# Kernel optimization log

Hardware: AMD Instinct MI355X
Metric: run time of the kernel (lower is better)

## Reference

```python
import jax, jax.numpy as jnp
import numpy as np

D_MODEL = 2048
H_TOTAL = 32
D_HEAD = D_MODEL // H_TOTAL  # 64
H_ACTIVE = 4
ROPE_BASE = 10000.0


def _apply_rope(t, cos, sin):
    # t: [B, H, T, DH]; cos/sin: [T, DH//2]; interleaved pair rotation
    t1 = t[..., 0::2]
    t2 = t[..., 1::2]
    r1 = t1 * cos - t2 * sin
    r2 = t1 * sin + t2 * cos
    return jnp.stack([r1, r2], axis=-1).reshape(t.shape)


def setup_inputs() -> dict:
    key = jax.random.key(0)
    ks = jax.random.split(key, 4)
    x = jax.random.normal(ks[0], (4, 1024, D_MODEL), dtype=jnp.float32)
    w_router = jax.random.normal(ks[1], (D_MODEL, H_TOTAL), dtype=jnp.float32) * 0.02
    w_qkv = jax.random.normal(ks[2], (D_MODEL, 3 * D_MODEL), dtype=jnp.float32) * 0.02
    w_out = jax.random.normal(ks[3], (D_MODEL, D_MODEL), dtype=jnp.float32) * 0.02
    return {"x": x, "w_router": w_router, "w_qkv": w_qkv, "w_out": w_out}


def reference(x, w_router, w_qkv, w_out):
    B, T, _ = x.shape
    # --- SwitchRouter: per-token probabilities over heads ---
    probs = jax.nn.softmax(x @ w_router, axis=-1)            # [B, T, H]
    # top-h_active heads per token (dense-math equivalent of sparse dispatch)
    _, top_idx = jax.lax.top_k(probs, H_ACTIVE)              # [B, T, HA]
    mask = jnp.sum(jax.nn.one_hot(top_idx, H_TOTAL, dtype=x.dtype), axis=-2)  # [B, T, H]
    gate = probs * mask                                      # router-scored gate

    # --- QKV projection ---
    qkv = x @ w_qkv                                          # [B, T, 3D]
    q, k, v = jnp.split(qkv, 3, axis=-1)
    def to_heads(t):
        return t.reshape(B, T, H_TOTAL, D_HEAD).transpose(0, 2, 1, 3)  # [B, H, T, DH]
    q, k, v = to_heads(q), to_heads(k), to_heads(v)

    # --- RoPE ---
    inv_freq = 1.0 / (ROPE_BASE ** (jnp.arange(0, D_HEAD, 2, dtype=jnp.float32) / D_HEAD))
    ang = jnp.arange(T, dtype=jnp.float32)[:, None] * inv_freq[None, :]  # [T, DH/2]
    cos, sin = jnp.cos(ang), jnp.sin(ang)
    q = _apply_rope(q, cos, sin)
    k = _apply_rope(k, cos, sin)

    # --- causal SDPA ---
    scores = jnp.einsum('bhqd,bhkd->bhqk', q, k) / np.float32(np.sqrt(D_HEAD))
    causal = jnp.tril(jnp.ones((T, T), dtype=bool))
    scores = jnp.where(causal, scores, jnp.finfo(scores.dtype).min)
    attn = jax.nn.softmax(scores, axis=-1)
    out = jnp.einsum('bhqk,bhkd->bhqd', attn, v)             # [B, H, T, DH]

    # --- gate: only active heads contribute (scatter-back equivalent) ---
    out = out * gate.transpose(0, 2, 1)[..., None]           # [B, H, T, DH]
    out = out.transpose(0, 2, 1, 3).reshape(B, T, D_MODEL)
    return out @ w_out
```

## Files before the change

kernel.cpp:

```cpp
#include <hip/hip_runtime.h>
#include <hip/hip_bf16.h>
#include <stdint.h>
#include <stddef.h>

typedef __attribute__((ext_vector_type(8))) short bf16x8;
typedef __attribute__((ext_vector_type(8))) unsigned short u16x8;
typedef __attribute__((ext_vector_type(4))) float f32x4;

#define TT 1024

__device__ __forceinline__ unsigned short f2bf(float f){
  unsigned u = __builtin_bit_cast(unsigned, f);
  unsigned r = 0x7fffu + ((u >> 16) & 1u);
  return (unsigned short)((u + r) >> 16);
}
__device__ __forceinline__ float bf2f(unsigned short s){
  unsigned u = ((unsigned)s) << 16;
  return __builtin_bit_cast(float, u);
}
__device__ __forceinline__ void gload16(const unsigned short* g, unsigned short* l){
  __builtin_amdgcn_global_load_lds(
      (const __attribute__((address_space(1))) void*)g,
      (__attribute__((address_space(3))) void*)l, 16, 0, 0);
}

__global__ void transpose_cast_kernel(const float* __restrict__ in, unsigned short* __restrict__ out,
                                      int R, int C){
  __shared__ float tile[32][33];
  int c0 = blockIdx.x * 32, r0 = blockIdx.y * 32;
  for (int i = threadIdx.y; i < 32; i += 8)
    tile[i][threadIdx.x] = in[(size_t)(r0 + i) * C + c0 + threadIdx.x];
  __syncthreads();
  for (int i = threadIdx.y; i < 32; i += 8)
    out[(size_t)(c0 + i) * R + r0 + threadIdx.x] = f2bf(tile[threadIdx.x][i]);
}

__global__ void rope_table_kernel(float* __restrict__ tab){
  int idx = blockIdx.x * 256 + threadIdx.x;
  int pos = idx >> 5, i = idx & 31;
  float freq = powf(10000.0f, -(float)i / 32.0f);
  float ang = (float)pos * freq;
  tab[idx * 2]     = cosf(ang);
  tab[idx * 2 + 1] = sinf(ang);
}

__global__ __launch_bounds__(256) void prep_kernel(const float* __restrict__ x,
                                                   const float* __restrict__ wr,
                                                   unsigned short* __restrict__ x_bf,
                                                   float* __restrict__ gate){
  __shared__ float xc[8 * 256];
  __shared__ float red[8 * 8 * 32];
  const int tid = threadIdx.x;
  const int tok0 = blockIdx.x * 8;
  const int p = tid >> 5, h = tid & 31;
  float acc[8] = {0.f,0.f,0.f,0.f,0.f,0.f,0.f,0.f};

  for (int kb = 0; kb < 8; kb++){
    __syncthreads();
    {
      int tok = tid >> 5, e = (tid & 31) * 8;
      const float* xp = x + (size_t)(tok0 + tok) * 2048 + kb * 256 + e;
      float4 v0 = *(const float4*)xp, v1 = *(const float4*)(xp + 4);
      float vals[8] = {v0.x, v0.y, v0.z, v0.w, v1.x, v1.y, v1.z, v1.w};
      u16x8 ob;
      #pragma unroll
      for (int jj = 0; jj < 8; jj++) ob[jj] = f2bf(vals[jj]);
      *(u16x8*)(x_bf + (size_t)(tok0 + tok) * 2048 + kb * 256 + e) = ob;
      #pragma unroll
      for (int jj = 0; jj < 8; jj++) xc[tok * 256 + e + jj] = vals[jj];
    }
    __syncthreads();
    const float* wp = wr + (size_t)(kb * 256 + p * 32) * 32 + h;
    #pragma unroll 4
    for (int j = 0; j < 32; j++){
      float wv = wp[j * 32];
      #pragma unroll
      for (int tok = 0; tok < 8; tok++)
        acc[tok] += xc[tok * 256 + p * 32 + j] * wv;
    }
  }
  #pragma unroll
  for (int tok = 0; tok < 8; tok++) red[(p * 8 + tok) * 32 + h] = acc[tok];
  __syncthreads();

  {
    int lane = tid & 63;
    int tok = (tid >> 6) * 2 + (lane >> 5);
    int hh = lane & 31;
    float logit = 0.f;
    #pragma unroll
    for (int pp = 0; pp < 8; pp++) logit += red[(pp * 8 + tok) * 32 + hh];
    float m = logit;
    #pragma unroll
    for (int s = 16; s >= 1; s >>= 1) m = fmaxf(m, __shfl_xor(m, s));
    float e = __expf(logit - m);
    float sum = e;
    #pragma unroll
    for (int s = 16; s >= 1; s >>= 1) sum += __shfl_xor(sum, s);
    float prob = e / sum;
    float v = logit; int sel = 0;
    #pragma unroll
    for (int rr2 = 0; rr2 < 4; rr2++){
      float bv = v; int bi = hh;
      #pragma unroll
      for (int s = 16; s >= 1; s >>= 1){
        float ov = __shfl_xor(bv, s); int oi = __shfl_xor(bi, s);
        if (ov > bv || (ov == bv && oi < bi)) { bv = ov; bi = oi; }
      }
      if (hh == bi) { sel = 1; v = -3.4e38f; }
    }
    gate[(size_t)(tok0 + tok) * 32 + hh] = sel ? prob : 0.f;
  }
}

__global__ void compact_kernel(const float* __restrict__ gate, int* __restrict__ idx,
                               int* __restrict__ counts){
  int bh = blockIdx.x;
  int b = bh >> 5, h = bh & 31;
  int lane = threadIdx.x;
  int base = 0;
  for (int c = 0; c < 16; c++){
    int t = c * 64 + lane;
    bool act = gate[(size_t)(b * TT + t) * 32 + h] != 0.f;
    unsigned long long mask = __ballot(act);
    int pos = base + __popcll(mask & ((1ull << lane) - 1ull));
    if (act) idx[bh * TT + pos] = t;
    base += __popcll(mask);
  }
  if (lane == 0) counts[bh] = base;
}

__global__ __launch_bounds__(256) void gemm_qkv(const unsigned short* __restrict__ A,
                                                const unsigned short* __restrict__ Bt,
                                                unsigned short* __restrict__ qk,
                                                unsigned short* __restrict__ vt,
                                                const float* __restrict__ tab){
  __shared__ unsigned short As[3][128 * 32];
  __shared__ unsigned short Bs[3][128 * 32];
  const int K = 2048;
  const int bn = blockIdx.x, bm = blockIdx.y;
  const int tid = threadIdx.x, lane = tid & 63, wid = tid >> 6;
  const int wr = wid >> 1, wc = wid & 1;
  const int li = lane & 15, lg = lane >> 4;

  const unsigned short* gA0 = A  + (size_t)(bm * 128 + (tid >> 2)) * K + (tid & 3) * 8;
  const unsigned short* gA1 = gA0 + (size_t)64 * K;
  const unsigned short* gB0 = Bt + (size_t)(bn * 128 + (tid >> 2)) * K + (tid & 3) * 8;
  const unsigned short* gB1 = gB0 + (size_t)64 * K;

  f32x4 acc[4][4];
  #pragma unroll
  for (int i = 0; i < 4; i++)
    #pragma unroll
    for (int j = 0; j < 4; j++) acc[i][j] = f32x4{0.f, 0.f, 0.f, 0.f};

  const int NT = K >> 5;
  #pragma unroll
  for (int pp = 0; pp < 2; pp++){
    int ko = pp * 32;
    gload16(gA0 + ko, &As[pp][tid * 8]);
    gload16(gA1 + ko, &As[pp][(256 + tid) * 8]);
    gload16(gB0 + ko, &Bs[pp][tid * 8]);
    gload16(gB1 + ko, &Bs[pp][(256 + tid) * 8]);
  }
  for (int t = 0; t < NT; ++t){
    if (t == NT - 1) asm volatile("s_waitcnt vmcnt(0)" ::: "memory");
    else             asm volatile("s_waitcnt vmcnt(4)" ::: "memory");
    __builtin_amdgcn_s_barrier();
    __builtin_amdgcn_sched_barrier(0);
    const int sl = t % 3;
    const unsigned short* as = &As[sl][0];
    const unsigned short* bs = &Bs[sl][0];
    bf16x8 af[4], bfr[4];
    #pragma unroll
    for (int i = 0; i < 4; i++){
      af[i]  = *(const bf16x8*)(as + (wr * 64 + i * 16 + li) * 32 + lg * 8);
      bfr[i] = *(const bf16x8*)(bs + (wc * 64 + i * 16 + li) * 32 + lg * 8);
    }
    if (t + 2 < NT){
      const int s2 = (t + 2) % 3;
      const int ko = (t + 2) * 32;
      gload16(gA0 + ko, &As[s2][tid * 8]);
      gload16(gA1 + ko, &As[s2][(256 + tid) * 8]);
      gload16(gB0 + ko, &Bs[s2][tid * 8]);
      gload16(gB1 + ko, &Bs[s2][(256 + tid) * 8]);
    }
    #pragma unroll
    for (int i = 0; i < 4; i++)
      #pragma unroll
      for (int j = 0; j < 4; j++)
        acc[i][j] = __builtin_amdgcn_mfma_f32_16x16x32_bf16(af[i], bfr[j], acc[i][j], 0, 0, 0);
  }

  if (bn < 32){
    #pragma unroll
    for (int i = 0; i < 4; i++){
      #pragma unroll
      for (int j = 0; j < 4; j++){
        int col = bn * 128 + wc * 64 + j * 16 + li;
        int ii = (col & 63) >> 1;
        #pragma unroll
        for (int r = 0; r < 4; r++){
          int row = bm * 128 + wr * 64 + i * 16 + lg * 4 + r;
          int pos = row & (TT - 1);
          const float* tp = tab + ((size_t)pos * 32 + ii) * 2;
          float c = tp[0], s = tp[1];
          float val = acc[i][j][r];
          float pv = __shfl_xor(val, 1);
          float res = (li & 1) ? (pv * s + val * c) : (val * c - pv * s);
          qk[(size_t)row * 4096 + col] = f2bf(res);
        }
      }
    }
  } else {
    #pragma unroll
    for (int i = 0; i < 4; i++){
      #pragma unroll
      for (int j = 0; j < 4; j++){
        int vcol = bn * 128 + wc * 64 + j * 16 + li - 4096;
        int hh = vcol >> 6, d = vcol & 63;
        int row0 = bm * 128 + wr * 64 + i * 16 + lg * 4;
        int b = row0 >> 10, t0 = row0 & (TT - 1);
        ushort4 pk;
        pk.x = f2bf(acc[i][j][0]); pk.y = f2bf(acc[i][j][1]);
        pk.z = f2bf(acc[i][j][2]); pk.w = f2bf(acc[i][j][3]);
        *(ushort4*)(vt + ((size_t)((b * 32 + hh) * 64 + d)) * TT + t0) = pk;
      }
    }
  }
}

__global__ __launch_bounds__(256) void gemm_out(const unsigned short* __restrict__ A,
                                                const unsigned short* __restrict__ Bt,
                                                float* __restrict__ C,
                                                int M, int N, int K){
  __shared__ unsigned short As[3][128 * 32];
  __shared__ unsigned short Bs[3][128 * 32];
  const int bn = blockIdx.x, bm = blockIdx.y;
  const int tid = threadIdx.x, lane = tid & 63, wid = tid >> 6;
  const int wr = wid >> 1, wc = wid & 1;
  const int li = lane & 15, lg = lane >> 4;
  const unsigned short* gA0 = A  + (size_t)(bm * 128 + (tid >> 2)) * K + (tid & 3) * 8;
  const unsigned short* gA1 = gA0 + (size_t)64 * K;
  const unsigned short* gB0 = Bt + (size_t)(bn * 128 + (tid >> 2)) * K + (tid & 3) * 8;
  const unsigned short* gB1 = gB0 + (size_t)64 * K;
  f32x4 acc[4][4];
  #pragma unroll
  for (int i = 0; i < 4; i++)
    #pragma unroll
    for (int j = 0; j < 4; j++) acc[i][j] = f32x4{0.f, 0.f, 0.f, 0.f};
  const int NT = K >> 5;
  #pragma unroll
  for (int pp = 0; pp < 2; pp++){
    int ko = pp * 32;
    gload16(gA0 + ko, &As[pp][tid * 8]);
    gload16(gA1 + ko, &As[pp][(256 + tid) * 8]);
    gload16(gB0 + ko, &Bs[pp][tid * 8]);
    gload16(gB1 + ko, &Bs[pp][(256 + tid) * 8]);
  }
  for (int t = 0; t < NT; ++t){
    if (t == NT - 1) asm volatile("s_waitcnt vmcnt(0)" ::: "memory");
    else             asm volatile("s_waitcnt vmcnt(4)" ::: "memory");
    __builtin_amdgcn_s_barrier();
    __builtin_amdgcn_sched_barrier(0);
    const int sl = t % 3;
    const unsigned short* as = &As[sl][0];
    const unsigned short* bs = &Bs[sl][0];
    bf16x8 af[4], bfr[4];
    #pragma unroll
    for (int i = 0; i < 4; i++){
      af[i]  = *(const bf16x8*)(as + (wr * 64 + i * 16 + li) * 32 + lg * 8);
      bfr[i] = *(const bf16x8*)(bs + (wc * 64 + i * 16 + li) * 32 + lg * 8);
    }
    if (t + 2 < NT){
      const int s2 = (t + 2) % 3;
      const int ko = (t + 2) * 32;
      gload16(gA0 + ko, &As[s2][tid * 8]);
      gload16(gA1 + ko, &As[s2][(256 + tid) * 8]);
      gload16(gB0 + ko, &Bs[s2][tid * 8]);
      gload16(gB1 + ko, &Bs[s2][(256 + tid) * 8]);
    }
    #pragma unroll
    for (int i = 0; i < 4; i++)
      #pragma unroll
      for (int j = 0; j < 4; j++)
        acc[i][j] = __builtin_amdgcn_mfma_f32_16x16x32_bf16(af[i], bfr[j], acc[i][j], 0, 0, 0);
  }
  #pragma unroll
  for (int i = 0; i < 4; i++)
    #pragma unroll
    for (int j = 0; j < 4; j++)
      #pragma unroll
      for (int r = 0; r < 4; r++){
        size_t row = (size_t)(bm * 128 + wr * 64 + i * 16 + lg * 4 + r);
        size_t col = (size_t)(bn * 128 + wc * 64 + j * 16 + li);
        C[row * N + col] = acc[i][j][r];
      }
}

__global__ __launch_bounds__(256) void attn_sparse_kernel(const unsigned short* __restrict__ qk,
                                                          const unsigned short* __restrict__ vt,
                                                          const float* __restrict__ gate,
                                                          const int* __restrict__ idx,
                                                          const int* __restrict__ counts,
                                                          unsigned short* __restrict__ attn_out){
  __shared__ unsigned short Ks[64 * 64];
  __shared__ unsigned short Vs[64 * 64];
  __shared__ unsigned short Ps[4][16 * 64];
  const int bh = blockIdx.x, qt = blockIdx.y;
  const int count = counts[bh];
  if (qt * 64 >= count) return;
  const int b = bh >> 5, h = bh & 31;
  const int tid = threadIdx.x, lane = tid & 63, w = tid >> 6;
  const int li = lane & 15, lg = lane >> 4;
  const int* myidx = idx + bh * TT + qt * 64;
  const int nvalid = min(64, count - qt * 64);
  const int qmax = myidx[nvalid - 1];

  int qi[4];
  #pragma unroll
  for (int r = 0; r < 4; r++){
    int s = w * 16 + lg * 4 + r;
    qi[r] = (s < nvalid) ? myidx[s] : -1;
  }
  int qrow = (w * 16 + li < nvalid) ? myidx[w * 16 + li] : 0;
  bf16x8 qf0, qf1;
  {
    const unsigned short* qp = qk + (size_t)(b * TT + qrow) * 4096 + h * 64;
    qf0 = *(const bf16x8*)(qp + lg * 8);
    qf1 = *(const bf16x8*)(qp + 32 + lg * 8);
  }
  f32x4 o[4];
  #pragma unroll
  for (int i = 0; i < 4; i++) o[i] = f32x4{0.f, 0.f, 0.f, 0.f};
  float m_run[4], l_run[4];
  #pragma unroll
  for (int r = 0; r < 4; r++){ m_run[r] = -1e30f; l_run[r] = 0.f; }

  const int nkt = (qmax >> 6) + 1;
  for (int kt = 0; kt < nkt; kt++){
    const int kb = kt * 64;
    #pragma unroll
    for (int s2 = 0; s2 < 2; s2++){
      int s = s2 * 256 + tid;
      int r = s >> 3, c = (s & 7) * 8;
      gload16(qk + (size_t)(b * TT + kb + r) * 4096 + 2048 + h * 64 + c, &Ks[s * 8]);
      gload16(vt + (size_t)(bh * 64 + r) * TT + kb + c, &Vs[s * 8]);
    }
    __syncthreads();

    f32x4 s4[4];
    #pragma unroll
    for (int ni = 0; ni < 4; ni++){
      bf16x8 k0 = *(const bf16x8*)(&Ks[(ni * 16 + li) * 64 + lg * 8]);
      bf16x8 k1 = *(const bf16x8*)(&Ks[(ni * 16 + li) * 64 + 32 + lg * 8]);
      f32x4 t = f32x4{0.f, 0.f, 0.f, 0.f};
      t = __builtin_amdgcn_mfma_f32_16x16x32_bf16(qf0, k0, t, 0, 0, 0);
      t = __builtin_amdgcn_mfma_f32_16x16x32_bf16(qf1, k1, t, 0, 0, 0);
      s4[ni] = t;
    }
    float mt[4];
    #pragma unroll
    for (int r = 0; r < 4; r++) mt[r] = -1e30f;
    #pragma unroll
    for (int ni = 0; ni < 4; ni++){
      int kidx = kb + ni * 16 + li;
      #pragma unroll
      for (int r = 0; r < 4; r++){
        float val = s4[ni][r] * 0.125f;
        val = (kidx <= qi[r]) ? val : -1e30f;
        s4[ni][r] = val;
        mt[r] = fmaxf(mt[r], val);
      }
    }
    #pragma unroll
    for (int r = 0; r < 4; r++){
      #pragma unroll
      for (int sh = 8; sh >= 1; sh >>= 1) mt[r] = fmaxf(mt[r], __shfl_xor(mt[r], sh));
      float mnew = fmaxf(m_run[r], mt[r]);
      float corr = __expf(m_run[r] - mnew);
      m_run[r] = mnew;
      l_run[r] *= corr;
      #pragma unroll
      for (int j = 0; j < 4; j++) o[j][r] *= corr;
    }
    float rs[4] = {0.f, 0.f, 0.f, 0.f};
    #pragma unroll
    for (int ni = 0; ni < 4; ni++)
      #pragma unroll
      for (int r = 0; r < 4; r++){
        float p = __expf(s4[ni][r] - m_run[r]);
        s4[ni][r] = p;
        rs[r] += p;
      }
    #pragma unroll
    for (int r = 0; r < 4; r++){
      #pragma unroll
      for (int sh = 8; sh >= 1; sh >>= 1) rs[r] += __shfl_xor(rs[r], sh);
      l_run[r] += rs[r];
    }
    #pragma unroll
    for (int ni = 0; ni < 4; ni++)
      #pragma unroll
      for (int r = 0; r < 4; r++)
        Ps[w][(lg * 4 + r) * 64 + ni * 16 + li] = f2bf(s4[ni][r]);
    #pragma unroll
    for (int ks = 0; ks < 2; ks++){
      bf16x8 pa = *(const bf16x8*)(&Ps[w][li * 64 + ks * 32 + lg * 8]);
      #pragma unroll
      for (int ni = 0; ni < 4; ni++){
        bf16x8 vb = *(const bf16x8*)(&Vs[(ni * 16 + li) * 64 + ks * 32 + lg * 8]);
        o[ni] = __builtin_amdgcn_mfma_f32_16x16x32_bf16(pa, vb, o[ni], 0, 0, 0);
      }
    }
    __syncthreads();
  }
  #pragma unroll
  for (int r = 0; r < 4; r++){
    if (qi[r] < 0) continue;
    float g = gate[(size_t)(b * TT + qi[r]) * 32 + h];
    float inv = g / l_run[r];
    #pragma unroll
    for (int ni = 0; ni < 4; ni++)
      attn_out[(size_t)(b * TT + qi[r]) * 2048 + h * 64 + ni * 16 + li] = f2bf(o[ni][r] * inv);
  }
}

extern "C" void kernel_launch(void* const* d_in, const int* in_sizes, int n_in,
                              void* d_out, int out_size, void* d_ws, size_t ws_size,
                              hipStream_t stream){
  const float* x        = (const float*)d_in[0];
  const float* w_router = (const float*)d_in[1];
  const float* w_qkv    = (const float*)d_in[2];
  const float* w_out    = (const float*)d_in[3];
  float* out = (float*)d_out;
  char* ws = (char*)d_ws;

  unsigned short* qk    = (unsigned short*)(ws);
  unsigned short* vt    = (unsigned short*)(ws + 33554432);
  unsigned short* x_bf  = (unsigned short*)(ws + 50331648);
  unsigned short* wqkvT = (unsigned short*)(ws + 67108864);
  unsigned short* woutT = (unsigned short*)(ws + 92274688);
  float* gate           = (float*)(ws + 100663296);
  float* tab            = (float*)(ws + 101187584);
  unsigned short* attn  = x_bf;
  int* idx              = (int*)(ws + 67108864);
  int* counts           = (int*)(ws + 67633152);

  hipLaunchKernelGGL(transpose_cast_kernel, dim3(192, 64), dim3(32, 8), 0, stream, w_qkv, wqkvT, 2048, 6144);
  hipLaunchKernelGGL(transpose_cast_kernel, dim3(64, 64), dim3(32, 8), 0, stream, w_out, woutT, 2048, 2048);
  hipLaunchKernelGGL(rope_table_kernel, dim3(128), dim3(256), 0, stream, tab);
  hipLaunchKernelGGL(prep_kernel, dim3(512), dim3(256), 0, stream, x, w_router, x_bf, gate);
  hipLaunchKernelGGL(gemm_qkv, dim3(48, 32), dim3(256), 0, stream, x_bf, wqkvT, qk, vt, tab);
  hipLaunchKernelGGL(compact_kernel, dim3(128), dim3(64), 0, stream, gate, idx, counts);
  hipMemsetAsync(attn, 0, (size_t)4096 * 2048 * 2, stream);
  hipLaunchKernelGGL(attn_sparse_kernel, dim3(128, 16), dim3(256), 0, stream, qk, vt, gate, idx, counts, attn);
  hipLaunchKernelGGL(gemm_out, dim3(16, 32), dim3(256), 0, stream, attn, woutT, out, 4096, 2048, 2048);
}
```

Before: 274.9 us.

## Replace both GEMMs with a 256x128-tile, 8-wave swizzled-LDS templated kernel

```diff
diff --git a/kernel.cpp b/kernel.cpp
--- a/kernel.cpp
+++ b/kernel.cpp
@@ -82,7 +82,6 @@
   #pragma unroll
   for (int tok = 0; tok < 8; tok++) red[(p * 8 + tok) * 32 + h] = acc[tok];
   __syncthreads();
-
   {
     int lane = tid & 63;
     int tok = (tid >> 6) * 2 + (lane >> 5);
@@ -130,23 +129,56 @@
   if (lane == 0) counts[bh] = base;
 }
 
-__global__ __launch_bounds__(256) void gemm_qkv(const unsigned short* __restrict__ A,
+#define MFMA_B16(a, b, c) __builtin_amdgcn_mfma_f32_16x16x32_bf16((a), (b), (c), 0, 0, 0)
+
+template<int EPI>
+__global__ __launch_bounds__(512, 2) void gemm8(const unsigned short* __restrict__ A,
                                                 const unsigned short* __restrict__ Bt,
+                                                float* __restrict__ Cf,
                                                 unsigned short* __restrict__ qk,
                                                 unsigned short* __restrict__ vt,
-                                                const float* __restrict__ tab){
-  __shared__ unsigned short As[3][128 * 32];
-  __shared__ unsigned short Bs[3][128 * 32];
-  const int K = 2048;
-  const int bn = blockIdx.x, bm = blockIdx.y;
+                                                const float* __restrict__ tab,
+                                                int N, int K, int nbn){
+  extern __shared__ unsigned short smem[];
+  unsigned short* SA = smem;
+  unsigned short* SB = smem + 49152;
+
+  const int nblk = gridDim.x;
+  int raw = blockIdx.x;
+  int tile = (raw & 7) * (nblk >> 3) + (raw >> 3);
+  const int bm = tile / nbn, bn = tile % nbn;
+
   const int tid = threadIdx.x, lane = tid & 63, wid = tid >> 6;
-  const int wr = wid >> 1, wc = wid & 1;
+  const int wrow = wid >> 1, wcol = wid & 1;
   const int li = lane & 15, lg = lane >> 4;
-
-  const unsigned short* gA0 = A  + (size_t)(bm * 128 + (tid >> 2)) * K + (tid & 3) * 8;
-  const unsigned short* gA1 = gA0 + (size_t)64 * K;
-  const unsigned short* gB0 = Bt + (size_t)(bn * 128 + (tid >> 2)) * K + (tid & 3) * 8;
-  const unsigned short* gB1 = gB0 + (size_t)64 * K;
+  const int swz = (li & 7) << 4;
+
+  const int aoff0 = (((wrow * 64 + li) * 128) + ((lg * 16) ^ swz)) >> 1;
+  const int aoff1 = (((wrow * 64 + li) * 128) + ((64 + lg * 16) ^ swz)) >> 1;
+  const int boff0 = (((wcol * 64 + li) * 128) + ((lg * 16) ^ swz)) >> 1;
+  const int boff1 = (((wcol * 64 + li) * 128) + ((64 + lg * 16) ^ swz)) >> 1;
+
+  int L0 = tid * 16,            r0_ = L0 >> 7, c0_ = (L0 & 127) ^ ((r0_ & 7) << 4);
+  int L1 = 8192 + tid * 16,     r1_ = L1 >> 7, c1_ = (L1 & 127) ^ ((r1_ & 7) << 4);
+  int L2 = 16384 + tid * 16,    r2_ = L2 >> 7, c2_ = (L2 & 127) ^ ((r2_ & 7) << 4);
+  int L3 = 24576 + tid * 16,    r3_ = L3 >> 7, c3_ = (L3 & 127) ^ ((r3_ & 7) << 4);
+  const unsigned short* gA0p = A + (size_t)(bm * 256 + r0_) * K + (c0_ >> 1);
+  const unsigned short* gA1p = A + (size_t)(bm * 256 + r1_) * K + (c1_ >> 1);
+  const unsigned short* gA2p = A + (size_t)(bm * 256 + r2_) * K + (c2_ >> 1);
+  const unsigned short* gA3p = A + (size_t)(bm * 256 + r3_) * K + (c3_ >> 1);
+  const unsigned short* gB0p = Bt + (size_t)(bn * 128 + r0_) * K + (c0_ >> 1);
+  const unsigned short* gB1p = Bt + (size_t)(bn * 128 + r1_) * K + (c1_ >> 1);
+  const int aL0 = L0 >> 1, aL1 = L1 >> 1, aL2 = L2 >> 1, aL3 = L3 >> 1;
+
+  auto stageA0 = [&](int tt){ unsigned short* b = SA + (tt % 3) * 16384;
+    gload16(gA0p + (size_t)tt * 64, b + aL0);
+    gload16(gA1p + (size_t)tt * 64, b + aL1); };
+  auto stageA1 = [&](int tt){ unsigned short* b = SA + (tt % 3) * 16384;
+    gload16(gA2p + (size_t)tt * 64, b + aL2);
+    gload16(gA3p + (size_t)tt * 64, b + aL3); };
+  auto stageB = [&](int tt){ unsigned short* b = SB + (tt % 3) * 8192;
+    gload16(gB0p + (size_t)tt * 64, b + aL0);
+    gload16(gB1p + (size_t)tt * 64, b + aL1); };
 
   f32x4 acc[4][4];
   #pragma unroll
@@ -154,148 +186,133 @@
     #pragma unroll
     for (int j = 0; j < 4; j++) acc[i][j] = f32x4{0.f, 0.f, 0.f, 0.f};
 
-  const int NT = K >> 5;
-  #pragma unroll
-  for (int pp = 0; pp < 2; pp++){
-    int ko = pp * 32;
-    gload16(gA0 + ko, &As[pp][tid * 8]);
-    gload16(gA1 + ko, &As[pp][(256 + tid) * 8]);
-    gload16(gB0 + ko, &Bs[pp][tid * 8]);
-    gload16(gB1 + ko, &Bs[pp][(256 + tid) * 8]);
-  }
+  const int NT = K >> 6;
+  stageA0(0); stageA1(0); stageB(0);
+  stageA0(1); stageA1(1); stageB(1);
+
   for (int t = 0; t < NT; ++t){
-    if (t == NT - 1) asm volatile("s_waitcnt vmcnt(0)" ::: "memory");
-    else             asm volatile("s_waitcnt vmcnt(4)" ::: "memory");
+    if (t < NT - 1) asm volatile("s_waitcnt vmcnt(6)" ::: "memory");
+    else            asm volatile("s_waitcnt vmcnt(0)" ::: "memory");
     __builtin_amdgcn_s_barrier();
     __builtin_amdgcn_sched_barrier(0);
-    const int sl = t % 3;
-    const unsigned short* as = &As[sl][0];
-    const unsigned short* bs = &Bs[sl][0];
-    bf16x8 af[4], bfr[4];
-    #pragma unroll
-    for (int i = 0; i < 4; i++){
-      af[i]  = *(const bf16x8*)(as + (wr * 64 + i * 16 + li) * 32 + lg * 8);
-      bfr[i] = *(const bf16x8*)(bs + (wc * 64 + i * 16 + li) * 32 + lg * 8);
-    }
-    if (t + 2 < NT){
-      const int s2 = (t + 2) % 3;
-      const int ko = (t + 2) * 32;
-      gload16(gA0 + ko, &As[s2][tid * 8]);
-      gload16(gA1 + ko, &As[s2][(256 + tid) * 8]);
-      gload16(gB0 + ko, &Bs[s2][tid * 8]);
-      gload16(gB1 + ko, &Bs[s2][(256 + tid) * 8]);
-    }
+    const unsigned short* as = SA + (t % 3) * 16384;
+    const unsigned short* bs = SB + (t % 3) * 8192;
+    const bool st = (t + 2 < NT);
+    bf16x8 a0, a1, a2, a3, b0, b1, b2, b3;
+
+    a0 = *(const bf16x8*)(as + aoff0);
+    a1 = *(const bf16x8*)(as + aoff0 + 1024);
+    b0 = *(const bf16x8*)(bs + boff0);
+    b1 = *(const bf16x8*)(bs + boff0 + 1024);
+    b2 = *(const bf16x8*)(bs + boff0 + 2048);
+    b3 = *(const bf16x8*)(bs + boff0 + 3072);
+    if (st) stageA0(t + 2);
+    __builtin_amdgcn_s_barrier();
+    asm volatile("s_waitcnt lgkmcnt(0)" ::: "memory");
+    __builtin_amdgcn_sched_barrier(0);
+    __builtin_amdgcn_s_setprio(1);
+    acc[0][0] = MFMA_B16(a0, b0, acc[0][0]); acc[0][1] = MFMA_B16(a0, b1, acc[0][1]);
+    acc[0][2] = MFMA_B16(a0, b2, acc[0][2]); acc[0][3] = MFMA_B16(a0, b3, acc[0][3]);
+    acc[1][0] = MFMA_B16(a1, b0, acc[1][0]); acc[1][1] = MFMA_B16(a1, b1, acc[1][1]);
+    acc[1][2] = MFMA_B16(a1, b2, acc[1][2]); acc[1][3] = MFMA_B16(a1, b3, acc[1][3]);
+    __builtin_amdgcn_s_setprio(0);
+    __builtin_amdgcn_s_barrier();
+
+    a2 = *(const bf16x8*)(as + aoff0 + 2048);
+    a3 = *(const bf16x8*)(as + aoff0 + 3072);
+    if (st) stageA1(t + 2);
+    __builtin_amdgcn_s_barrier();
+    asm volatile("s_waitcnt lgkmcnt(0)" ::: "memory");
+    __builtin_amdgcn_sched_barrier(0);
+    __builtin_amdgcn_s_setprio(1);
+    acc[2][0] = MFMA_B16(a2, b0, acc[2][0]); acc[2][1] = MFMA_B16(a2, b1, acc[2][1]);
+    acc[2][2] = MFMA_B16(a2, b2, acc[2][2]); acc[2][3] = MFMA_B16(a2, b3, acc[2][3]);
+    acc[3][0] = MFMA_B16(a3, b0, acc[3][0]); acc[3][1] = MFMA_B16(a3, b1, acc[3][1]);
+    acc[3][2] = MFMA_B16(a3, b2, acc[3][2]); acc[3][3] = MFMA_B16(a3, b3, acc[3][3]);
+    __builtin_amdgcn_s_setprio(0);
+    __builtin_amdgcn_s_barrier();
+
+    a0 = *(const bf16x8*)(as + aoff1);
+    a1 = *(const bf16x8*)(as + aoff1 + 1024);
+    b0 = *(const bf16x8*)(bs + boff1);
+    b1 = *(const bf16x8*)(bs + boff1 + 1024);
+    b2 = *(const bf16x8*)(bs + boff1 + 2048);
+    b3 = *(const bf16x8*)(bs + boff1 + 3072);
+    if (st) stageB(t + 2);
+    __builtin_amdgcn_s_barrier();
+    asm volatile("s_waitcnt lgkmcnt(0)" ::: "memory");
+    __builtin_amdgcn_sched_barrier(0);
+    __builtin_amdgcn_s_setprio(1);
+    acc[0][0] = MFMA_B16(a0, b0, acc[0][0]); acc[0][1] = MFMA_B16(a0, b1, acc[0][1]);
+    acc[0][2] = MFMA_B16(a0, b2, acc[0][2]); acc[0][3] = MFMA_B16(a0, b3, acc[0][3]);
+    acc[1][0] = MFMA_B16(a1, b0, acc[1][0]); acc[1][1] = MFMA_B16(a1, b1, acc[1][1]);
+    acc[1][2] = MFMA_B16(a1, b2, acc[1][2]); acc[1][3] = MFMA_B16(a1, b3, acc[1][3]);
+    __builtin_amdgcn_s_setprio(0);
+    __builtin_amdgcn_s_barrier();
+
+    a2 = *(const bf16x8*)(as + aoff1 + 2048);
+    a3 = *(const bf16x8*)(as + aoff1 + 3072);
+    __builtin_amdgcn_s_barrier();
+    asm volatile("s_waitcnt lgkmcnt(0)" ::: "memory");
+    __builtin_amdgcn_sched_barrier(0);
+    __builtin_amdgcn_s_setprio(1);
+    acc[2][0] = MFMA_B16(a2, b0, acc[2][0]); acc[2][1] = MFMA_B16(a2, b1, acc[2][1]);
+    acc[2][2] = MFMA_B16(a2, b2, acc[2][2]); acc[2][3] = MFMA_B16(a2, b3, acc[2][3]);
+    acc[3][0] = MFMA_B16(a3, b0, acc[3][0]); acc[3][1] = MFMA_B16(a3, b1, acc[3][1]);
+    acc[3][2] = MFMA_B16(a3, b2, acc[3][2]); acc[3][3] = MFMA_B16(a3, b3, acc[3][3]);
+    __builtin_amdgcn_s_setprio(0);
+  }
+
+  if (EPI == 1){
+    const int colbase = bn * 128 + wcol * 64;
+    if (bn < 32){
+      #pragma unroll
+      for (int i = 0; i < 4; i++){
+        #pragma unroll
+        for (int j = 0; j < 4; j++){
+          int col = colbase + j * 16 + li;
+          int ii = (col & 63) >> 1;
+          #pragma unroll
+          for (int r = 0; r < 4; r++){
+            int row = bm * 256 + wrow * 64 + i * 16 + lg * 4 + r;
+            int pos = row & (TT - 1);
+            const float* tp = tab + ((size_t)pos * 32 + ii) * 2;
+            float c = tp[0], s = tp[1];
+            float val = acc[i][j][r];
+            float pv = __shfl_xor(val, 1);
+            float res = (li & 1) ? (pv * s + val * c) : (val * c - pv * s);
+            qk[(size_t)row * 4096 + col] = f2bf(res);
+          }
+        }
+      }
+    } else {
+      #pragma unroll
+      for (int i = 0; i < 4; i++){
+        #pragma unroll
+        for (int j = 0; j < 4; j++){
+          int vcol = colbase + j * 16 + li - 4096;
+          int hh = vcol >> 6, d = vcol & 63;
+          int row0 = bm * 256 + wrow * 64 + i * 16 + lg * 4;
+          int b = row0 >> 10, t0 = row0 & (TT - 1);
+          ushort4 pk;
+          pk.x = f2bf(acc[i][j][0]); pk.y = f2bf(acc[i][j][1]);
+          pk.z = f2bf(acc[i][j][2]); pk.w = f2bf(acc[i][j][3]);
+          *(ushort4*)(vt + ((size_t)((b * 32 + hh) * 64 + d)) * TT + t0) = pk;
+        }
+      }
+    }
+  } else {
     #pragma unroll
     for (int i = 0; i < 4; i++)
       #pragma unroll
       for (int j = 0; j < 4; j++)
-        acc[i][j] = __builtin_amdgcn_mfma_f32_16x16x32_bf16(af[i], bfr[j], acc[i][j], 0, 0, 0);
-  }
-
-  if (bn < 32){
-    #pragma unroll
-    for (int i = 0; i < 4; i++){
-      #pragma unroll
-      for (int j = 0; j < 4; j++){
-        int col = bn * 128 + wc * 64 + j * 16 + li;
-        int ii = (col & 63) >> 1;
         #pragma unroll
         for (int r = 0; r < 4; r++){
-          int row = bm * 128 + wr * 64 + i * 16 + lg * 4 + r;
-          int pos = row & (TT - 1);
-          const float* tp = tab + ((size_t)pos * 32 + ii) * 2;
-          float c = tp[0], s = tp[1];
-          float val = acc[i][j][r];
-          float pv = __shfl_xor(val, 1);
-          float res = (li & 1) ? (pv * s + val * c) : (val * c - pv * s);
-          qk[(size_t)row * 4096 + col] = f2bf(res);
+          size_t row = (size_t)(bm * 256 + wrow * 64 + i * 16 + lg * 4 + r);
+          size_t col = (size_t)(bn * 128 + wcol * 64 + j * 16 + li);
+          Cf[row * N + col] = acc[i][j][r];
         }
-      }
-    }
-  } else {
-    #pragma unroll
-    for (int i = 0; i < 4; i++){
-      #pragma unroll
-      for (int j = 0; j < 4; j++){
-        int vcol = bn * 128 + wc * 64 + j * 16 + li - 4096;
-        int hh = vcol >> 6, d = vcol & 63;
-        int row0 = bm * 128 + wr * 64 + i * 16 + lg * 4;
-        int b = row0 >> 10, t0 = row0 & (TT - 1);
-        ushort4 pk;
-        pk.x = f2bf(acc[i][j][0]); pk.y = f2bf(acc[i][j][1]);
-        pk.z = f2bf(acc[i][j][2]); pk.w = f2bf(acc[i][j][3]);
-        *(ushort4*)(vt + ((size_t)((b * 32 + hh) * 64 + d)) * TT + t0) = pk;
-      }
-    }
-  }
-}
-
-__global__ __launch_bounds__(256) void gemm_out(const unsigned short* __restrict__ A,
-                                                const unsigned short* __restrict__ Bt,
-                                                float* __restrict__ C,
-                                                int M, int N, int K){
-  __shared__ unsigned short As[3][128 * 32];
-  __shared__ unsigned short Bs[3][128 * 32];
-  const int bn = blockIdx.x, bm = blockIdx.y;
-  const int tid = threadIdx.x, lane = tid & 63, wid = tid >> 6;
-  const int wr = wid >> 1, wc = wid & 1;
-  const int li = lane & 15, lg = lane >> 4;
-  const unsigned short* gA0 = A  + (size_t)(bm * 128 + (tid >> 2)) * K + (tid & 3) * 8;
-  const unsigned short* gA1 = gA0 + (size_t)64 * K;
-  const unsigned short* gB0 = Bt + (size_t)(bn * 128 + (tid >> 2)) * K + (tid & 3) * 8;
-  const unsigned short* gB1 = gB0 + (size_t)64 * K;
-  f32x4 acc[4][4];
-  #pragma unroll
-  for (int i = 0; i < 4; i++)
-    #pragma unroll
-    for (int j = 0; j < 4; j++) acc[i][j] = f32x4{0.f, 0.f, 0.f, 0.f};
-  const int NT = K >> 5;
-  #pragma unroll
-  for (int pp = 0; pp < 2; pp++){
-    int ko = pp * 32;
-    gload16(gA0 + ko, &As[pp][tid * 8]);
-    gload16(gA1 + ko, &As[pp][(256 + tid) * 8]);
-    gload16(gB0 + ko, &Bs[pp][tid * 8]);
-    gload16(gB1 + ko, &Bs[pp][(256 + tid) * 8]);
-  }
-  for (int t = 0; t < NT; ++t){
-    if (t == NT - 1) asm volatile("s_waitcnt vmcnt(0)" ::: "memory");
-    else             asm volatile("s_waitcnt vmcnt(4)" ::: "memory");
-    __builtin_amdgcn_s_barrier();
-    __builtin_amdgcn_sched_barrier(0);
-    const int sl = t % 3;
-    const unsigned short* as = &As[sl][0];
-    const unsigned short* bs = &Bs[sl][0];
-    bf16x8 af[4], bfr[4];
-    #pragma unroll
-    for (int i = 0; i < 4; i++){
-      af[i]  = *(const bf16x8*)(as + (wr * 64 + i * 16 + li) * 32 + lg * 8);
-      bfr[i] = *(const bf16x8*)(bs + (wc * 64 + i * 16 + li) * 32 + lg * 8);
-    }
-    if (t + 2 < NT){
-      const int s2 = (t + 2) % 3;
-      const int ko = (t + 2) * 32;
-      gload16(gA0 + ko, &As[s2][tid * 8]);
-      gload16(gA1 + ko, &As[s2][(256 + tid) * 8]);
-      gload16(gB0 + ko, &Bs[s2][tid * 8]);
-      gload16(gB1 + ko, &Bs[s2][(256 + tid) * 8]);
-    }
-    #pragma unroll
-    for (int i = 0; i < 4; i++)
-      #pragma unroll
-      for (int j = 0; j < 4; j++)
-        acc[i][j] = __builtin_amdgcn_mfma_f32_16x16x32_bf16(af[i], bfr[j], acc[i][j], 0, 0, 0);
-  }
-  #pragma unroll
-  for (int i = 0; i < 4; i++)
-    #pragma unroll
-    for (int j = 0; j < 4; j++)
-      #pragma unroll
-      for (int r = 0; r < 4; r++){
-        size_t row = (size_t)(bm * 128 + wr * 64 + i * 16 + lg * 4 + r);
-        size_t col = (size_t)(bn * 128 + wc * 64 + j * 16 + li);
-        C[row * N + col] = acc[i][j][r];
-      }
+  }
 }
 
 __global__ __launch_bounds__(256) void attn_sparse_kernel(const unsigned short* __restrict__ qk,
@@ -355,8 +372,8 @@
       bf16x8 k0 = *(const bf16x8*)(&Ks[(ni * 16 + li) * 64 + lg * 8]);
       bf16x8 k1 = *(const bf16x8*)(&Ks[(ni * 16 + li) * 64 + 32 + lg * 8]);
       f32x4 t = f32x4{0.f, 0.f, 0.f, 0.f};
-      t = __builtin_amdgcn_mfma_f32_16x16x32_bf16(qf0, k0, t, 0, 0, 0);
-      t = __builtin_amdgcn_mfma_f32_16x16x32_bf16(qf1, k1, t, 0, 0, 0);
+      t = MFMA_B16(qf0, k0, t);
+      t = MFMA_B16(qf1, k1, t);
       s4[ni] = t;
     }
     float mt[4];
@@ -410,7 +427,7 @@
       #pragma unroll
       for (int ni = 0; ni < 4; ni++){
         bf16x8 vb = *(const bf16x8*)(&Vs[(ni * 16 + li) * 64 + ks * 32 + lg * 8]);
-        o[ni] = __builtin_amdgcn_mfma_f32_16x16x32_bf16(pa, vb, o[ni], 0, 0, 0);
+        o[ni] = MFMA_B16(pa, vb, o[ni]);
       }
     }
     __syncthreads();
@@ -447,13 +464,22 @@
   int* idx              = (int*)(ws + 67108864);
   int* counts           = (int*)(ws + 67633152);
 
+  constexpr int GEMM_LDS = 147456;
+  (void)hipFuncSetAttribute(reinterpret_cast<const void*>(&gemm8<1>),
+                            hipFuncAttributeMaxDynamicSharedMemorySize, GEMM_LDS);
+  (void)hipFuncSetAttribute(reinterpret_cast<const void*>(&gemm8<0>),
+                            hipFuncAttributeMaxDynamicSharedMemorySize, GEMM_LDS);
+
   hipLaunchKernelGGL(transpose_cast_kernel, dim3(192, 64), dim3(32, 8), 0, stream, w_qkv, wqkvT, 2048, 6144);
   hipLaunchKernelGGL(transpose_cast_kernel, dim3(64, 64), dim3(32, 8), 0, stream, w_out, woutT, 2048, 2048);
   hipLaunchKernelGGL(rope_table_kernel, dim3(128), dim3(256), 0, stream, tab);
   hipLaunchKernelGGL(prep_kernel, dim3(512), dim3(256), 0, stream, x, w_router, x_bf, gate);
-  hipLaunchKernelGGL(gemm_qkv, dim3(48, 32), dim3(256), 0, stream, x_bf, wqkvT, qk, vt, tab);
+  hipLaunchKernelGGL((gemm8<1>), dim3(768), dim3(512), GEMM_LDS, stream,
+                     x_bf, wqkvT, (float*)nullptr, qk, vt, tab, 6144, 2048, 48);
   hipLaunchKernelGGL(compact_kernel, dim3(128), dim3(64), 0, stream, gate, idx, counts);
-  hipMemsetAsync(attn, 0, (size_t)4096 * 2048 * 2, stream);
+  (void)hipMemsetAsync(attn, 0, (size_t)4096 * 2048 * 2, stream);
   hipLaunchKernelGGL(attn_sparse_kernel, dim3(128, 16), dim3(256), 0, stream, qk, vt, gate, idx, counts, attn);
-  hipLaunchKernelGGL(gemm_out, dim3(16, 32), dim3(256), 0, stream, attn, woutT, out, 4096, 2048, 2048);
-}
+  hipLaunchKernelGGL((gemm8<0>), dim3(256), dim3(512), GEMM_LDS, stream,
+                     attn, woutT, out, (unsigned short*)nullptr, (unsigned short*)nullptr,
+                     (const float*)nullptr, 2048, 2048, 16);
+}
```

New measurement: 262.8 us. 1.05x faster.
